# Kernel optimization log

Measured on AMD Instinct MI355X. Metric: run time of the kernel, lower is better.

## Reference

```python
import jax, jax.numpy as jnp
import numpy as np

S, T, B = 1024, 64, 8
KEY_DIM, QUERY_DIM, HIDDEN = 512, 512, 256


def setup_inputs() -> dict:
    key = jax.random.key(0)
    ks = jax.random.split(key, 8)
    inp = {
        "key": jax.random.normal(ks[0], (S, B, KEY_DIM), dtype=jnp.float32),
        "query": jax.random.normal(ks[1], (T, B, QUERY_DIM), dtype=jnp.float32),
        # torch nn.Linear params, stored as (in, out) for x @ W
        "Wk": jax.random.normal(ks[2], (KEY_DIM, HIDDEN), dtype=jnp.float32) * (1.0 / np.sqrt(KEY_DIM)),
        "bk": jax.random.normal(ks[3], (HIDDEN,), dtype=jnp.float32) * 0.01,
        "Wq": jax.random.normal(ks[4], (QUERY_DIM, HIDDEN), dtype=jnp.float32) * (1.0 / np.sqrt(QUERY_DIM)),
        "bq": jax.random.normal(ks[5], (HIDDEN,), dtype=jnp.float32) * 0.01,
        "v": jax.random.normal(ks[6], (HIDDEN,), dtype=jnp.float32),
    }
    return inp


def reference(key, query, Wk, bk, Wq, bq, v):
    # key: (S, B, Dk), query: (T, B, Dq)
    key_proj = key @ Wk + bk          # (S, B, H)
    query_proj = query @ Wq + bq      # (T, B, H)
    # broadcast add: (T,1,B,H) + (1,S,B,H) -> (T,S,B,H)
    energy = jnp.tanh(query_proj[:, None, :, :] + key_proj[None, :, :, :])
    scores = jnp.einsum('tsbh,h->tsb', energy, v)  # (T, S, B)
    attn = jax.nn.softmax(scores, axis=1)          # softmax over key positions S
    return jnp.transpose(attn, (2, 0, 1))          # (B, T, S)
```

## Files before the change

### kernel.cpp

```cpp
#include <hip/hip_runtime.h>

#define S_DIM 1024
#define T_DIM 64
#define B_DIM 8
#define K_DIM 512
#define H_DIM 256

typedef _Float16 f16;
typedef __attribute__((ext_vector_type(4))) _Float16 f16x4;
typedef __attribute__((ext_vector_type(8))) _Float16 f16x8;
typedef __attribute__((ext_vector_type(4))) float f32x4;

__device__ __forceinline__ float fast_rcp(float x) { return __builtin_amdgcn_rcpf(x); }

__device__ __forceinline__ void gload16(const void* g, void* l) {
    __builtin_amdgcn_global_load_lds(
        (const __attribute__((address_space(1))) unsigned int*)g,
        (__attribute__((address_space(3))) unsigned int*)l, 16, 0, 0);
}

__global__ __launch_bounds__(256) void wconv_kernel(
    const float* __restrict__ Wk, const float* __restrict__ Wq,
    f16* __restrict__ WTk, f16* __restrict__ WTq)
{
    __shared__ float tile[64][65];
    const int idx = blockIdx.x;
    const float* W = (idx & 32) ? Wq : Wk;
    f16* WT = (idx & 32) ? WTq : WTk;
    const int t32 = idx & 31;
    const int k0 = (t32 >> 2) * 64, n0 = (t32 & 3) * 64;
    const int c = threadIdx.x & 63, r0 = threadIdx.x >> 6;
#pragma unroll
    for (int i = 0; i < 16; ++i) {
        int r = r0 + i * 4;
        tile[r][c] = W[(size_t)(k0 + r) * H_DIM + n0 + c];
    }
    __syncthreads();
#pragma unroll
    for (int i = 0; i < 16; ++i) {
        int r = r0 + i * 4;
        WT[(size_t)(n0 + r) * K_DIM + k0 + c] = (f16)tile[c][r];
    }
}

__global__ __launch_bounds__(256, 4) void proj_gemm_all(
    const float* __restrict__ key, const f16* __restrict__ WTk,
    const float* __restrict__ bk, float* __restrict__ ktT,
    const float* __restrict__ query, const f16* __restrict__ WTq,
    const float* __restrict__ bq, float* __restrict__ tq2)
{
    __shared__ __align__(16) char smem[2][16384];
    const int tid = threadIdx.x;
    const int lane = tid & 63, wid = tid >> 6;
    const int widu = __builtin_amdgcn_readfirstlane(wid);
    const int wm = (wid >> 1) * 16, wn = (wid & 1) * 32;

    const int bid0 = blockIdx.x;
    const int bid = (bid0 & 7) * 136 + (bid0 >> 3);
    const bool isQ = bid >= 1024;
    const int lb = isQ ? bid - 1024 : bid;
    const size_t m0 = (size_t)(lb >> 2) * 32;
    const int n0 = (lb & 3) * 64;
    const float* A    = isQ ? query : key;
    const f16* BT     = isQ ? WTq : WTk;
    const float* bias = isQ ? bq : bk;

    const int o0 = tid << 4;
    const int o1 = o0 + 4096;
    const int row0 = o0 >> 7, kb0 = (o0 & 127) ^ ((row0 & 7) << 4);
    const int row1 = o1 >> 7, kb1 = (o1 & 127) ^ ((row1 & 7) << 4);
    const char* b_t = (const char*)(BT + (size_t)n0 * K_DIM);

    auto GLOADB = [&](int buf, int t) {
        const int kb = t * 128;
        char* d0 = &smem[buf][8192 + widu * 1024];
        gload16(b_t + (size_t)row0 * 1024 + kb + kb0, d0);
        gload16(b_t + (size_t)row1 * 1024 + kb + kb1, d0 + 4096);
    };

    const float* a_base = A + m0 * K_DIM;
    float4 areg[2];
    auto ALOAD = [&](int t) {
#pragma unroll
        for (int j = 0; j < 2; ++j) {
            const int fidx = j * 256 + tid;
            const int r = fidx >> 4, c16 = fidx & 15;
            areg[j] = *(const float4*)&a_base[(size_t)r * K_DIM + t * 64 + c16 * 4];
        }
    };
    auto AWRITE = [&](int buf) {
#pragma unroll
        for (int j = 0; j < 2; ++j) {
            const int fidx = j * 256 + tid;
            const int r = fidx >> 4, c16 = fidx & 15;
            const int byt = r * 128 + ((c16 * 8) ^ ((r & 7) << 4));
            f16 h0 = (f16)areg[j].x, h1 = (f16)areg[j].y, h2 = (f16)areg[j].z, h3 = (f16)areg[j].w;
            f16x4 hi = {h0, h1, h2, h3};
            f16x4 lo = {(f16)(areg[j].x - (float)h0), (f16)(areg[j].y - (float)h1),
                        (f16)(areg[j].z - (float)h2), (f16)(areg[j].w - (float)h3)};
            *(f16x4*)&smem[buf][byt] = hi;
            *(f16x4*)&smem[buf][4096 + byt] = lo;
        }
    };

    f32x4 acc[2] = {};
    const int fr = lane & 15, fgb = (lane >> 4) << 4;

    auto COMPUTE = [&](int buf) {
#pragma unroll
        for (int kk = 0; kk < 2; ++kk) {
            const int kbyte = kk * 64 + fgb;
            const int arow = wm + fr;
            const int abyt = (arow << 7) + (kbyte ^ ((arow & 7) << 4));
            f16x8 ah = *(const f16x8*)&smem[buf][abyt];
            f16x8 al = *(const f16x8*)&smem[buf][4096 + abyt];
            const int brow0 = wn + fr, brow1 = wn + 16 + fr;
            f16x8 b0 = *(const f16x8*)&smem[buf][8192 + (brow0 << 7) + (kbyte ^ ((brow0 & 7) << 4))];
            f16x8 b1 = *(const f16x8*)&smem[buf][8192 + (brow1 << 7) + (kbyte ^ ((brow1 & 7) << 4))];
            acc[0] = __builtin_amdgcn_mfma_f32_16x16x32_f16(ah, b0, acc[0], 0, 0, 0);
            acc[1] = __builtin_amdgcn_mfma_f32_16x16x32_f16(ah, b1, acc[1], 0, 0, 0);
            acc[0] = __builtin_amdgcn_mfma_f32_16x16x32_f16(al, b0, acc[0], 0, 0, 0);
            acc[1] = __builtin_amdgcn_mfma_f32_16x16x32_f16(al, b1, acc[1], 0, 0, 0);
        }
    };

    ALOAD(0);
    GLOADB(0, 0);
    AWRITE(0);
    __syncthreads();

    int buf = 0;
#pragma unroll 1
    for (int t = 0; t < 8; ++t) {
        if (t < 7) {
            ALOAD(t + 1);
            GLOADB(buf ^ 1, t + 1);
        }
        COMPUTE(buf);
        if (t < 7) {
            AWRITE(buf ^ 1);
            __syncthreads();
        }
        buf ^= 1;
    }

    const int crow = (lane >> 4) * 4, ccol = lane & 15;
    if (isQ) {
#pragma unroll
        for (int g = 0; g < 2; ++g) {
            int col = n0 + wn + g * 16 + ccol;
            float bv = bias[col];
#pragma unroll
            for (int r = 0; r < 4; ++r) {
                size_t row = m0 + wm + crow + r;
                float val = __expf(2.0f * (acc[g][r] + bv));
                tq2[((size_t)(row & 7) * T_DIM + (row >> 3)) * H_DIM + col] = val;
            }
        }
    } else {
        float* lt = (float*)&smem[0][0];
#pragma unroll
        for (int g = 0; g < 2; ++g) {
            int lcol = wn + g * 16 + ccol;
            float bv = bias[n0 + lcol];
#pragma unroll
            for (int r = 0; r < 4; ++r) {
                int lrow = wm + crow + r;
                lt[lrow * 64 + lcol] = __expf(2.0f * (acc[g][r] + bv));
            }
        }
        __syncthreads();
        const int sbase = (int)(m0 >> 3);
        const int n0q = n0 >> 2;
#pragma unroll
        for (int p = 0; p < 2; ++p) {
            int c = p * 256 + tid;
            int s_off = c & 3, h4 = (c >> 2) & 15, b2 = c >> 6;
            float4 o = *(const float4*)&lt[(s_off * 8 + b2) * 64 + h4 * 4];
            size_t f4idx = ((size_t)b2 * 64 + n0q + h4) * S_DIM + sbase + s_off;
            *(float4*)&ktT[f4idx * 4] = o;
        }
    }
}

__global__ __launch_bounds__(256) void scores_kernel(
    const float* __restrict__ ktT, const float* __restrict__ tq2,
    const float* __restrict__ v, float* __restrict__ scores)
{
    const int tid = threadIdx.x, lane = tid & 63;
    const int wid = __builtin_amdgcn_readfirstlane(tid >> 6);
    const int bb = blockIdx.x;
    const int b = bb & 7;
    const int sblk = (bb >> 3) & 15;
    const int t0 = ((bb >> 7) << 3) + wid * 2;
    const int s = sblk * 64 + lane;

    const float4* kb4 = (const float4*)ktT + (size_t)b * 64 * S_DIM + s;
    const float* q0p = tq2 + ((size_t)b * T_DIM + t0) * H_DIM;
    const float* q1p = q0p + H_DIM;
    float* so = scores + ((size_t)b * T_DIM + t0) * S_DIM + s;

    float a0 = 0.f, a1 = 0.f;
#pragma unroll 8
    for (int h4 = 0; h4 < H_DIM / 4; ++h4) {
        float4 k4 = kb4[(size_t)h4 * S_DIM];
        float4 vv = *(const float4*)&v[h4 * 4];
        float4 q0 = *(const float4*)&q0p[h4 * 4];
        float4 q1 = *(const float4*)&q1p[h4 * 4];
        float A, B;
        A = fmaf(q0.x, k4.x, 1.0f); B = fmaf(q0.y, k4.y, 1.0f);
        a0 = fmaf(fmaf(vv.x, B, vv.y * A), fast_rcp(A * B), a0);
        A = fmaf(q0.z, k4.z, 1.0f); B = fmaf(q0.w, k4.w, 1.0f);
        a0 = fmaf(fmaf(vv.z, B, vv.w * A), fast_rcp(A * B), a0);
        A = fmaf(q1.x, k4.x, 1.0f); B = fmaf(q1.y, k4.y, 1.0f);
        a1 = fmaf(fmaf(vv.x, B, vv.y * A), fast_rcp(A * B), a1);
        A = fmaf(q1.z, k4.z, 1.0f); B = fmaf(q1.w, k4.w, 1.0f);
        a1 = fmaf(fmaf(vv.z, B, vv.w * A), fast_rcp(A * B), a1);
    }
    so[0]     = -2.0f * a0;
    so[S_DIM] = -2.0f * a1;
}

__global__ __launch_bounds__(256) void softmax_kernel(
    const float* __restrict__ scores, float* __restrict__ out)
{
    const int row = blockIdx.x;
    const int lane = threadIdx.x & 63;
    const int wave = threadIdx.x >> 6;
    __shared__ float red[8];

    float4 x = ((const float4*)(scores + (size_t)row * S_DIM))[threadIdx.x];
    float m = fmaxf(fmaxf(x.x, x.y), fmaxf(x.z, x.w));
#pragma unroll
    for (int mm = 32; mm >= 1; mm >>= 1) m = fmaxf(m, __shfl_xor(m, mm, 64));
    if (lane == 0) red[wave] = m;
    __syncthreads();
    m = fmaxf(fmaxf(red[0], red[1]), fmaxf(red[2], red[3]));

    float e0 = __expf(x.x - m), e1 = __expf(x.y - m);
    float e2 = __expf(x.z - m), e3 = __expf(x.w - m);
    float sum = e0 + e1 + e2 + e3;
#pragma unroll
    for (int mm = 32; mm >= 1; mm >>= 1) sum += __shfl_xor(sum, mm, 64);
    if (lane == 0) red[4 + wave] = sum;
    __syncthreads();
    float inv = fast_rcp(red[4] + red[5] + red[6] + red[7]);

    float4 o;
    o.x = e0 * inv; o.y = e1 * inv; o.z = e2 * inv; o.w = e3 * inv;
    ((float4*)(out + (size_t)row * S_DIM))[threadIdx.x] = o;
}

extern "C" void kernel_launch(void* const* d_in, const int* in_sizes, int n_in,
                              void* d_out, int out_size, void* d_ws, size_t ws_size,
                              hipStream_t stream)
{
    const float* key   = (const float*)d_in[0];
    const float* query = (const float*)d_in[1];
    const float* Wk    = (const float*)d_in[2];
    const float* bk    = (const float*)d_in[3];
    const float* Wq    = (const float*)d_in[4];
    const float* bq    = (const float*)d_in[5];
    const float* v     = (const float*)d_in[6];
    float* out = (float*)d_out;

    float* ktT    = (float*)d_ws;
    float* tq2    = ktT + (size_t)B_DIM * H_DIM * S_DIM;
    float* scores = tq2 + (size_t)B_DIM * T_DIM * H_DIM;
    f16* WTk = (f16*)(scores + (size_t)B_DIM * T_DIM * S_DIM);
    f16* WTq = WTk + (size_t)H_DIM * K_DIM;

    wconv_kernel<<<64, 256, 0, stream>>>(Wk, Wq, WTk, WTq);
    proj_gemm_all<<<1088, 256, 0, stream>>>(key, WTk, bk, ktT, query, WTq, bq, tq2);
    scores_kernel<<<1024, 256, 0, stream>>>(ktT, tq2, v, scores);
    softmax_kernel<<<B_DIM * T_DIM, 256, 0, stream>>>(scores, out);
}
```

Before: 45.61 us.

## Fuse scores and softmax into one kernel with full-row blocks

Merges the scores and softmax kernels so each 1024-thread block computes two full score rows over all key positions and normalizes them in-register with block reductions. This removes the intermediate scores buffer round trip and one kernel launch. In exchange, each block now reuses key projections across only two query rows instead of eight, which increases reads of the transposed key tensor, and launches fewer, larger blocks.

Result: faster. 44.13 us (median of 2 runs) (-3.2%).

```diff
diff --git a/kernel.cpp b/kernel.cpp
--- a/kernel.cpp
+++ b/kernel.cpp
@@ -183,22 +183,21 @@
     }
 }
 
-__global__ __launch_bounds__(256) void scores_kernel(
+__global__ __launch_bounds__(1024) void scores_softmax_kernel(
     const float* __restrict__ ktT, const float* __restrict__ tq2,
-    const float* __restrict__ v, float* __restrict__ scores)
-{
+    const float* __restrict__ v, float* __restrict__ out)
+{
+    __shared__ float redm[2][16], reds[2][16];
     const int tid = threadIdx.x, lane = tid & 63;
     const int wid = __builtin_amdgcn_readfirstlane(tid >> 6);
-    const int bb = blockIdx.x;
-    const int b = bb & 7;
-    const int sblk = (bb >> 3) & 15;
-    const int t0 = ((bb >> 7) << 3) + wid * 2;
-    const int s = sblk * 64 + lane;
+    const int bid = blockIdx.x;
+    const int b = bid & 7;
+    const int t0 = (bid >> 3) * 2;
+    const int s = tid;
 
     const float4* kb4 = (const float4*)ktT + (size_t)b * 64 * S_DIM + s;
     const float* q0p = tq2 + ((size_t)b * T_DIM + t0) * H_DIM;
     const float* q1p = q0p + H_DIM;
-    float* so = scores + ((size_t)b * T_DIM + t0) * S_DIM + s;
 
     float a0 = 0.f, a1 = 0.f;
 #pragma unroll 8
@@ -217,38 +216,40 @@
         A = fmaf(q1.z, k4.z, 1.0f); B = fmaf(q1.w, k4.w, 1.0f);
         a1 = fmaf(fmaf(vv.z, B, vv.w * A), fast_rcp(A * B), a1);
     }
-    so[0]     = -2.0f * a0;
-    so[S_DIM] = -2.0f * a1;
-}
-
-__global__ __launch_bounds__(256) void softmax_kernel(
-    const float* __restrict__ scores, float* __restrict__ out)
-{
-    const int row = blockIdx.x;
-    const int lane = threadIdx.x & 63;
-    const int wave = threadIdx.x >> 6;
-    __shared__ float red[8];
-
-    float4 x = ((const float4*)(scores + (size_t)row * S_DIM))[threadIdx.x];
-    float m = fmaxf(fmaxf(x.x, x.y), fmaxf(x.z, x.w));
-#pragma unroll
-    for (int mm = 32; mm >= 1; mm >>= 1) m = fmaxf(m, __shfl_xor(m, mm, 64));
-    if (lane == 0) red[wave] = m;
-    __syncthreads();
-    m = fmaxf(fmaxf(red[0], red[1]), fmaxf(red[2], red[3]));
-
-    float e0 = __expf(x.x - m), e1 = __expf(x.y - m);
-    float e2 = __expf(x.z - m), e3 = __expf(x.w - m);
-    float sum = e0 + e1 + e2 + e3;
-#pragma unroll
-    for (int mm = 32; mm >= 1; mm >>= 1) sum += __shfl_xor(sum, mm, 64);
-    if (lane == 0) red[4 + wave] = sum;
-    __syncthreads();
-    float inv = fast_rcp(red[4] + red[5] + red[6] + red[7]);
-
-    float4 o;
-    o.x = e0 * inv; o.y = e1 * inv; o.z = e2 * inv; o.w = e3 * inv;
-    ((float4*)(out + (size_t)row * S_DIM))[threadIdx.x] = o;
+    a0 *= -2.0f;
+    a1 *= -2.0f;
+
+    float m0 = a0, m1 = a1;
+#pragma unroll
+    for (int mm = 32; mm >= 1; mm >>= 1) {
+        m0 = fmaxf(m0, __shfl_xor(m0, mm, 64));
+        m1 = fmaxf(m1, __shfl_xor(m1, mm, 64));
+    }
+    if (lane == 0) { redm[0][wid] = m0; redm[1][wid] = m1; }
+    __syncthreads();
+    m0 = redm[0][0]; m1 = redm[1][0];
+#pragma unroll
+    for (int i = 1; i < 16; ++i) {
+        m0 = fmaxf(m0, redm[0][i]);
+        m1 = fmaxf(m1, redm[1][i]);
+    }
+
+    float e0 = __expf(a0 - m0), e1 = __expf(a1 - m1);
+    float s0 = e0, s1 = e1;
+#pragma unroll
+    for (int mm = 32; mm >= 1; mm >>= 1) {
+        s0 += __shfl_xor(s0, mm, 64);
+        s1 += __shfl_xor(s1, mm, 64);
+    }
+    if (lane == 0) { reds[0][wid] = s0; reds[1][wid] = s1; }
+    __syncthreads();
+    s0 = 0.f; s1 = 0.f;
+#pragma unroll
+    for (int i = 0; i < 16; ++i) { s0 += reds[0][i]; s1 += reds[1][i]; }
+
+    float* o = out + ((size_t)b * T_DIM + t0) * S_DIM + s;
+    o[0]     = e0 * fast_rcp(s0);
+    o[S_DIM] = e1 * fast_rcp(s1);
 }
 
 extern "C" void kernel_launch(void* const* d_in, const int* in_sizes, int n_in,
@@ -266,12 +267,10 @@
 
     float* ktT    = (float*)d_ws;
     float* tq2    = ktT + (size_t)B_DIM * H_DIM * S_DIM;
-    float* scores = tq2 + (size_t)B_DIM * T_DIM * H_DIM;
-    f16* WTk = (f16*)(scores + (size_t)B_DIM * T_DIM * S_DIM);
+    f16* WTk = (f16*)(tq2 + (size_t)B_DIM * T_DIM * H_DIM);
     f16* WTq = WTk + (size_t)H_DIM * K_DIM;
 
     wconv_kernel<<<64, 256, 0, stream>>>(Wk, Wq, WTk, WTq);
     proj_gemm_all<<<1088, 256, 0, stream>>>(key, WTk, bk, ktT, query, WTq, bq, tq2);
-    scores_kernel<<<1024, 256, 0, stream>>>(ktT, tq2, v, scores);
-    softmax_kernel<<<B_DIM * T_DIM, 256, 0, stream>>>(scores, out);
-}
+    scores_softmax_kernel<<<256, 1024, 0, stream>>>(ktT, tq2, v, out);
+}
```
